# Performance work log

Hardware: AMD Instinct MI355X
Metric: run time of the kernel (lower is better)

The kernel has to match this reference:

```python
import jax, jax.numpy as jnp
import numpy as np

D_MODEL = 1024
D_FF = 4096
N_HEADS = 16
HEAD_DIM = D_MODEL // N_HEADS
EPS = 1e-6
B, S = 4, 2048


def _linear_params(key, d_in, d_out):
    kw, kb = jax.random.split(key)
    scale = 1.0 / np.sqrt(d_in)
    w = jax.random.uniform(kw, (d_in, d_out), minval=-scale, maxval=scale, dtype=jnp.float32)
    b = jax.random.uniform(kb, (d_out,), minval=-scale, maxval=scale, dtype=jnp.float32)
    return w, b


def setup_inputs() -> dict:
    key = jax.random.key(0)
    ks = jax.random.split(key, 16)
    x = jax.random.normal(ks[0], (B, S, D_MODEL), dtype=jnp.float32)
    enc = jax.random.normal(ks[1], (B, S, D_MODEL), dtype=jnp.float32)
    # masked self-attention params
    wq1, bq1 = _linear_params(ks[2], D_MODEL, D_MODEL)
    wk1, bk1 = _linear_params(ks[3], D_MODEL, D_MODEL)
    wv1, bv1 = _linear_params(ks[4], D_MODEL, D_MODEL)
    wo1, bo1 = _linear_params(ks[5], D_MODEL, D_MODEL)
    # cross-attention params
    wq2, bq2 = _linear_params(ks[6], D_MODEL, D_MODEL)
    wk2, bk2 = _linear_params(ks[7], D_MODEL, D_MODEL)
    wv2, bv2 = _linear_params(ks[8], D_MODEL, D_MODEL)
    wo2, bo2 = _linear_params(ks[9], D_MODEL, D_MODEL)
    # feed-forward params
    wf1, bf1 = _linear_params(ks[10], D_MODEL, D_FF)
    wf2, bf2 = _linear_params(ks[11], D_FF, D_MODEL)
    # layer norms
    g1 = jnp.ones((D_MODEL,), jnp.float32); be1 = jnp.zeros((D_MODEL,), jnp.float32)
    g2 = jnp.ones((D_MODEL,), jnp.float32); be2 = jnp.zeros((D_MODEL,), jnp.float32)
    g3 = jnp.ones((D_MODEL,), jnp.float32); be3 = jnp.zeros((D_MODEL,), jnp.float32)
    return dict(x=x, encoder_output=enc,
                wq1=wq1, bq1=bq1, wk1=wk1, bk1=bk1, wv1=wv1, bv1=bv1, wo1=wo1, bo1=bo1,
                wq2=wq2, bq2=bq2, wk2=wk2, bk2=bk2, wv2=wv2, bv2=bv2, wo2=wo2, bo2=bo2,
                wf1=wf1, bf1=bf1, wf2=wf2, bf2=bf2,
                g1=g1, be1=be1, g2=g2, be2=be2, g3=g3, be3=be3)


def _layer_norm(x, g, b):
    mu = jnp.mean(x, axis=-1, keepdims=True)
    var = jnp.mean(jnp.square(x - mu), axis=-1, keepdims=True)
    return (x - mu) * jax.lax.rsqrt(var + EPS) * g + b


def _mha(q_in, k_in, v_in, wq, bq, wk, bk, wv, bv, wo, bo, causal):
    b, s, _ = q_in.shape
    q = (q_in @ wq + bq).reshape(b, s, N_HEADS, HEAD_DIM)
    k = (k_in @ wk + bk).reshape(b, -1, N_HEADS, HEAD_DIM)
    v = (v_in @ wv + bv).reshape(b, -1, N_HEADS, HEAD_DIM)
    scores = jnp.einsum('bqhd,bkhd->bhqk', q, k) / np.sqrt(HEAD_DIM)
    if causal:
        mask = jnp.tril(jnp.ones((s, s), dtype=bool))
        scores = jnp.where(mask, scores, jnp.finfo(scores.dtype).min)
    attn = jax.nn.softmax(scores, axis=-1)
    out = jnp.einsum('bhqk,bkhd->bqhd', attn, v).reshape(b, s, D_MODEL)
    return out @ wo + bo


def reference(x, encoder_output,
              wq1, bq1, wk1, bk1, wv1, bv1, wo1, bo1,
              wq2, bq2, wk2, bk2, wv2, bv2, wo2, bo2,
              wf1, bf1, wf2, bf2,
              g1, be1, g2, be2, g3, be3):
    # masked self-attention + residual + LN
    residual = x
    x = _mha(x, x, x, wq1, bq1, wk1, bk1, wv1, bv1, wo1, bo1, causal=True)
    x = _layer_norm(x + residual, g1, be1)
    # cross-attention (note: q=enc, k=enc, v=x as in the original) + residual + LN
    residual = x
    x = _mha(encoder_output, encoder_output, x, wq2, bq2, wk2, bk2, wv2, bv2, wo2, bo2, causal=False)
    x = _layer_norm(x + residual, g2, be2)
    # feed-forward (dropout=0 -> identity in eval) + residual + LN
    residual = x
    x = jax.nn.relu(x @ wf1 + bf1) @ wf2 + bf2
    x = _layer_norm(x + residual, g3, be3)
    return x
```

## Files before the change

### kernel.cpp

```cpp
#include <hip/hip_runtime.h>


typedef _Float16 f16;
typedef _Float16 f16x8 __attribute__((ext_vector_type(8)));
typedef _Float16 f16x4 __attribute__((ext_vector_type(4)));
typedef __fp16 fp16x2 __attribute__((ext_vector_type(2)));
typedef float f32x4 __attribute__((ext_vector_type(4)));
typedef float f32x16 __attribute__((ext_vector_type(16)));
typedef unsigned int u32;

#define AS1 __attribute__((address_space(1)))
#define AS3 __attribute__((address_space(3)))

constexpr int S_LEN = 2048;
constexpr int DM    = 1024;

constexpr long OFF_W    = 0;
constexpr long OFF_XB   = 32L  << 20;
constexpr long OFF_ENC  = 48L  << 20;
constexpr long OFF_Q    = 64L  << 20;
constexpr long OFF_K    = 80L  << 20;
constexpr long OFF_V    = 96L  << 20;
constexpr long OFF_VT   = 112L << 20;
constexpr long OFF_AC   = 128L << 20;
constexpr long OFF_HID  = 144L << 20;
constexpr long OFF_F1   = 208L << 20;
constexpr long OFF_F2   = 240L << 20;
constexpr long OFF_F3   = 272L << 20;
constexpr long OFF_PART = 304L << 20;
constexpr long BUF_BYTES = 336L << 20;

__device__ alignas(4096) unsigned char g_buf[BUF_BYTES];

constexpr long WQ1T = OFF_W + (0L  << 20);
constexpr long WF1T = OFF_W + (16L << 20);
constexpr long WF2T = OFF_W + (24L << 20);
constexpr long WO1T = OFF_W + (6L  << 20);
constexpr long WQ2T = OFF_W + (8L  << 20);
constexpr long WV2T = OFF_W + (12L << 20);
constexpr long WO2T = OFF_W + (14L << 20);

__global__ __launch_bounds__(256) void cvt2_k(const float* __restrict__ x,
                                              const float* __restrict__ enc)
{
    const int bid = blockIdx.x;
    const bool second = bid >= 8192;
    const float* in = second ? enc : x;
    f16* out = (f16*)(g_buf + (second ? OFF_ENC : OFF_XB));
    long i = (long)(second ? bid - 8192 : bid) * 256 + threadIdx.x;
    float4 v = ((const float4*)in)[i];
    f16x4 h;
    h.x = (f16)v.x; h.y = (f16)v.y; h.z = (f16)v.z; h.w = (f16)v.w;
    *(f16x4*)(out + i * 4) = h;
}

struct TWJobs { const float* src[10]; };

__global__ __launch_bounds__(256) void transw_all_k(TWJobs jobs)
{
    __shared__ float t[32][33];
    const int bid = blockIdx.x;
    int j, local;
    if (bid < 8192)       { j = bid >> 10; local = bid & 1023; }
    else if (bid < 12288) { j = 8; local = bid - 8192; }
    else                  { j = 9; local = bid - 12288; }
    const int K = (j == 9) ? 4096 : 1024;
    const int N = (j == 8) ? 4096 : 1024;
    const int tnx = N >> 5;
    const int tx32 = local % tnx, ty32 = local / tnx;
    const long dstOff = (j < 8) ? (long)j * (2L << 20) : ((j == 8) ? WF1T : WF2T);
    const float* W = jobs.src[j];
    f16* Wt = (f16*)(g_buf + dstOff);

    int tx = threadIdx.x, ty = threadIdx.y;
    int c0 = tx32 * 32, r0 = ty32 * 32;
#pragma unroll
    for (int i = 0; i < 4; ++i)
        t[ty + 8*i][tx] = W[(long)(r0 + ty + 8*i) * N + c0 + tx];
    __syncthreads();
#pragma unroll
    for (int i = 0; i < 4; ++i)
        Wt[(long)(c0 + ty + 8*i) * K + r0 + tx] = (f16)t[tx][ty + 8*i];
}

template<int MODE>
__global__ __launch_bounds__(256) void gemm3_k(
    long aOff, long bOff, long cOff, long vtOff,
    const float* __restrict__ b0, const float* __restrict__ b1,
    const float* __restrict__ b2, const float* __restrict__ b3,
    int K, int lda, int ldb, int ldc, long chunkStride, int tvch)
{
    __shared__ alignas(16) f16 As[3][128 * 32];
    __shared__ alignas(16) f16 Bs[3][128 * 32];

    const int tid  = threadIdx.x;
    const int lane = tid & 63;
    const int w    = tid >> 6;
    const int cB   = lane & 15;
    const int hi   = lane >> 4;

    const int nwg = gridDim.x * gridDim.y;
    const int id  = blockIdx.y * gridDim.x + blockIdx.x;
    const int swz = (id & 7) * (nwg >> 3) + (id >> 3);
    const int bx  = swz % gridDim.x, by = swz / gridDim.x;
    const int row0 = by * 128, col0 = bx * 128;

    const f16* Ab = (const f16*)(g_buf + aOff);
    const f16* Bb = (const f16*)(g_buf + bOff);

    const int wr = (w >> 1) * 64;
    const int wc = (w & 1) * 64;

    f32x4 acc[4][4] = {};

    auto stage = [&](int buf, int kt) {
        const int kB = kt * 32;
        const int base = w * 64;
#pragma unroll
        for (int r = 0; r < 2; ++r) {
            const int idx  = r * 256 + base + lane;
            const int srow = idx >> 2, sb = idx & 3;
            const int gk = (sb ^ ((srow >> 1) & 3)) << 3;
            __builtin_amdgcn_global_load_lds(
                (const AS1 void*)(Ab + (long)(row0 + srow) * lda + kB + gk),
                (AS3 void*)(&As[buf][(r * 256 + base) * 8]), 16, 0, 0);
            __builtin_amdgcn_global_load_lds(
                (const AS1 void*)(Bb + (long)(col0 + srow) * ldb + kB + gk),
                (AS3 void*)(&Bs[buf][(r * 256 + base) * 8]), 16, 0, 0);
        }
    };

    const int nt = K >> 5;
    stage(0, 0);
    stage(1, 1);

    for (int t = 0; t < nt; ++t) {
        if (nt - t >= 2) asm volatile("s_waitcnt vmcnt(4)" ::: "memory");
        else             asm volatile("s_waitcnt vmcnt(0)" ::: "memory");
        __builtin_amdgcn_s_barrier();
        __builtin_amdgcn_sched_barrier(0);
        if (t + 2 < nt) stage((t + 2) % 3, t + 2);

        const int cur = t % 3;
        f16x8 af[4], bf[4];
#pragma unroll
        for (int m = 0; m < 4; ++m) {
            const int row = wr + m * 16 + cB;
            af[m] = *(const f16x8*)&As[cur][row * 32 + ((hi ^ ((row >> 1) & 3)) << 3)];
        }
#pragma unroll
        for (int n = 0; n < 4; ++n) {
            const int row = wc + n * 16 + cB;
            bf[n] = *(const f16x8*)&Bs[cur][row * 32 + ((hi ^ ((row >> 1) & 3)) << 3)];
        }
        __builtin_amdgcn_s_setprio(1);
#pragma unroll
        for (int m = 0; m < 4; ++m)
#pragma unroll
            for (int n = 0; n < 4; ++n)
                acc[m][n] = __builtin_amdgcn_mfma_f32_16x16x32_f16(af[m], bf[n], acc[m][n], 0, 0, 0);
        __builtin_amdgcn_s_setprio(0);
    }

    const int ch = col0 >> 10;
    const float* bp = (ch == 0) ? b0 : (ch == 1) ? b1 : (ch == 2) ? b2 : b3;

    if (MODE == 0 && ch == tvch) {
        f16* Vt = (f16*)(g_buf + vtOff);
#pragma unroll
        for (int m = 0; m < 4; ++m) {
#pragma unroll
            for (int n = 0; n < 4; ++n) {
                const int c = col0 + wc + n * 16 + cB;
                const int hh = (c >> 6) & 15, dd = c & 63;
                const float bv = bp[c & 1023];
                const int r0e = row0 + wr + m * 16 + hi * 4;
                const int bb = r0e >> 11, sS = r0e & 2047;
                f16x4 hv;
#pragma unroll
                for (int jj = 0; jj < 4; ++jj) hv[jj] = (f16)(acc[m][n][jj] + bv);
                *(f16x4*)(Vt + (((long)(bb * 16 + hh) * 64 + dd) * 2048 + sS)) = hv;
            }
        }
        return;
    }

    float* Cf = (float*)(g_buf + cOff);
    f16*  Ch = (f16*)(g_buf + cOff);
    const long cBase = (long)ch * chunkStride;
#pragma unroll
    for (int m = 0; m < 4; ++m) {
#pragma unroll
        for (int n = 0; n < 4; ++n) {
            const int c = col0 + wc + n * 16 + cB;
            const float bv = bp[c & 1023];
#pragma unroll
            for (int jj = 0; jj < 4; ++jj) {
                const int r = row0 + wr + m * 16 + hi * 4 + jj;
                float v = acc[m][n][jj] + bv;
                const long idx = cBase + (long)r * ldc + (c & 1023);
                if constexpr (MODE == 2) Cf[idx] = v;
                else                     Ch[idx] = (f16)v;
            }
        }
    }
}

template<int MODE>
__global__ __launch_bounds__(512, 1) void gemm8_k(
    long aOff, long bOff, long cOff, long partOff, long vtOff,
    const float* __restrict__ b0, const float* __restrict__ b1,
    const float* __restrict__ b2, const float* __restrict__ b3,
    int K, int lda, int ldb, int ldc, long chunkStride, int tvch)
{
    __shared__ alignas(16) f16 As[2][2][8192];
    __shared__ alignas(16) f16 Bs[2][2][8192];

    const int tid  = threadIdx.x;
    const int lane = tid & 63;
    const int w    = tid >> 6;
    const int cB   = lane & 15;
    const int hi   = lane >> 4;

    const int gx = gridDim.x, gy = gridDim.y;
    const int nwg = gx * gy * gridDim.z;
    const int id  = ((int)blockIdx.z * gy + (int)blockIdx.y) * gx + (int)blockIdx.x;
    const int swz = (id & 7) * (nwg >> 3) + (id >> 3);
    const int bx  = swz % gx;
    const int rem = swz / gx;
    const int by  = rem % gy;
    const int bz  = rem / gy;
    const int row0 = by * 256, col0 = bx * 256;

    const f16* Ab = (const f16*)(g_buf + aOff) + (long)bz * K;
    const f16* Bb = (const f16*)(g_buf + bOff) + (long)bz * K;

    const int wr = (w >> 2) * 128;
    const int wc = (w & 3) * 64;

    f32x4 acc[8][4] = {};

    auto stagePlane = [&](int buf, int kt, int mat, int kh) {
        const int kB = kt * 64 + kh * 32;
        const f16* src = mat ? Bb : Ab;
        const int ld   = mat ? ldb : lda;
        const int r0g  = mat ? col0 : row0;
        f16* dst = mat ? &Bs[buf][kh][0] : &As[buf][kh][0];
#pragma unroll
        for (int r = 0; r < 2; ++r) {
            const int idx  = r * 512 + w * 64 + lane;
            const int srow = idx >> 2, sb = idx & 3;
            const int gk = (sb ^ ((srow >> 1) & 3)) << 3;
            __builtin_amdgcn_global_load_lds(
                (const AS1 void*)(src + (long)(r0g + srow) * ld + kB + gk),
                (AS3 void*)(dst + (r * 512 + w * 64) * 8), 16, 0, 0);
        }
    };

    auto rdA = [&](int buf, int kh, int mf) -> f16x8 {
        const int row = wr + mf * 16 + cB;
        return *(const f16x8*)&As[buf][kh][row * 32 + ((hi ^ ((row >> 1) & 3)) << 3)];
    };
    auto rdB = [&](int buf, int kh, int nf) -> f16x8 {
        const int row = wc + nf * 16 + cB;
        return *(const f16x8*)&Bs[buf][kh][row * 32 + ((hi ^ ((row >> 1) & 3)) << 3)];
    };

    const int nt = K >> 6;
    stagePlane(0, 0, 0, 0);
    stagePlane(0, 0, 1, 0);
    stagePlane(0, 0, 0, 1);
    stagePlane(0, 0, 1, 1);

    for (int t = 0; t < nt; ++t) {
        const int cur = t & 1, nxt = cur ^ 1;
        const bool pf = (t + 1 < nt);
        f16x8 a[4], b[4];

        asm volatile("s_waitcnt vmcnt(4)" ::: "memory");
        __builtin_amdgcn_s_barrier();
        __builtin_amdgcn_sched_barrier(0);
#pragma unroll
        for (int n = 0; n < 4; ++n) b[n] = rdB(cur, 0, n);
#pragma unroll
        for (int m = 0; m < 4; ++m) a[m] = rdA(cur, 0, m);
        if (pf) stagePlane(nxt, t + 1, 0, 0);
        asm volatile("s_waitcnt lgkmcnt(0)" ::: "memory");
        __builtin_amdgcn_sched_barrier(0);
        __builtin_amdgcn_s_setprio(1);
#pragma unroll
        for (int m = 0; m < 4; ++m)
#pragma unroll
            for (int n = 0; n < 4; ++n)
                acc[m][n] = __builtin_amdgcn_mfma_f32_16x16x32_f16(a[m], b[n], acc[m][n], 0, 0, 0);
        __builtin_amdgcn_s_setprio(0);

        __builtin_amdgcn_s_barrier();
        __builtin_amdgcn_sched_barrier(0);
#pragma unroll
        for (int m = 0; m < 4; ++m) a[m] = rdA(cur, 0, m + 4);
        if (pf) stagePlane(nxt, t + 1, 1, 0);
        asm volatile("s_waitcnt lgkmcnt(0)" ::: "memory");
        __builtin_amdgcn_sched_barrier(0);
        __builtin_amdgcn_s_setprio(1);
#pragma unroll
        for (int m = 0; m < 4; ++m)
#pragma unroll
            for (int n = 0; n < 4; ++n)
                acc[4 + m][n] = __builtin_amdgcn_mfma_f32_16x16x32_f16(a[m], b[n], acc[4 + m][n], 0, 0, 0);
        __builtin_amdgcn_s_setprio(0);

        if (pf) asm volatile("s_waitcnt vmcnt(4)" ::: "memory");
        else    asm volatile("s_waitcnt vmcnt(0)" ::: "memory");
        __builtin_amdgcn_s_barrier();
        __builtin_amdgcn_sched_barrier(0);
#pragma unroll
        for (int n = 0; n < 4; ++n) b[n] = rdB(cur, 1, n);
#pragma unroll
        for (int m = 0; m < 4; ++m) a[m] = rdA(cur, 1, m);
        if (pf) stagePlane(nxt, t + 1, 0, 1);
        asm volatile("s_waitcnt lgkmcnt(0)" ::: "memory");
        __builtin_amdgcn_sched_barrier(0);
        __builtin_amdgcn_s_setprio(1);
#pragma unroll
        for (int m = 0; m < 4; ++m)
#pragma unroll
            for (int n = 0; n < 4; ++n)
                acc[m][n] = __builtin_amdgcn_mfma_f32_16x16x32_f16(a[m], b[n], acc[m][n], 0, 0, 0);
        __builtin_amdgcn_s_setprio(0);

        __builtin_amdgcn_s_barrier();
        __builtin_amdgcn_sched_barrier(0);
#pragma unroll
        for (int m = 0; m < 4; ++m) a[m] = rdA(cur, 1, m + 4);
        if (pf) stagePlane(nxt, t + 1, 1, 1);
        asm volatile("s_waitcnt lgkmcnt(0)" ::: "memory");
        __builtin_amdgcn_sched_barrier(0);
        __builtin_amdgcn_s_setprio(1);
#pragma unroll
        for (int m = 0; m < 4; ++m)
#pragma unroll
            for (int n = 0; n < 4; ++n)
                acc[4 + m][n] = __builtin_amdgcn_mfma_f32_16x16x32_f16(a[m], b[n], acc[4 + m][n], 0, 0, 0);
        __builtin_amdgcn_s_setprio(0);
    }

    const int ch = col0 >> 10;
    const float* bp = (ch == 0) ? b0 : (ch == 1) ? b1 : (ch == 2) ? b2 : b3;

    if (MODE == 0 && ch == tvch) {
        f16* Vt = (f16*)(g_buf + vtOff);
#pragma unroll
        for (int m = 0; m < 8; ++m) {
#pragma unroll
            for (int n = 0; n < 4; ++n) {
                const int c = col0 + wc + n * 16 + cB;
                const int hh = (c >> 6) & 15, dd = c & 63;
                const float bv = bp[c & 1023];
                const int r0e = row0 + wr + m * 16 + hi * 4;
                const int bb = r0e >> 11, sS = r0e & 2047;
                f16x4 hv;
#pragma unroll
                for (int jj = 0; jj < 4; ++jj) hv[jj] = (f16)(acc[m][n][jj] + bv);
                *(f16x4*)(Vt + (((long)(bb * 16 + hh) * 64 + dd) * 2048 + sS)) = hv;
            }
        }
        return;
    }

    float* Cf = (float*)(g_buf + (bz ? partOff : cOff));
    f16*  Ch = (f16*)(g_buf + cOff);
    const long cBase = (long)ch * chunkStride;
#pragma unroll
    for (int m = 0; m < 8; ++m) {
#pragma unroll
        for (int n = 0; n < 4; ++n) {
            const int c = col0 + wc + n * 16 + cB;
            const float bv = bz ? 0.f : bp[c & 1023];
#pragma unroll
            for (int jj = 0; jj < 4; ++jj) {
                const int r = row0 + wr + m * 16 + hi * 4 + jj;
                float v = acc[m][n][jj] + bv;
                if constexpr (MODE == 1) v = fmaxf(v, 0.f);
                const long idx = cBase + (long)r * ldc + (c & 1023);
                if constexpr (MODE == 2) Cf[idx] = v;
                else                     Ch[idx] = (f16)v;
            }
        }
    }
}

template<int CAUSAL>
__global__ __launch_bounds__(256, 4) void flash_k(long qOff, long kOff, long vtOff, long oOff)
{
    __shared__ alignas(16) f16 KV[2][2][4096];

    const int tid  = threadIdx.x;
    const int lane = tid & 63;
    const int w    = tid >> 6;
    const int ql   = lane & 31;
    const int s    = lane >> 5;

    int bh, pairIdx = 0, qtSingle = 0;
    if (CAUSAL) {
        const int raw   = (int)blockIdx.y * (int)gridDim.x + (int)blockIdx.x;
        const int newid = (raw & 7) * 64 + (raw >> 3);
        bh = newid >> 3; pairIdx = newid & 7;
    } else {
        const int raw   = (int)blockIdx.y * (int)gridDim.x + (int)blockIdx.x;
        const int newid = (raw & 7) * 128 + (raw >> 3);
        bh = newid >> 4; qtSingle = newid & 15;
    }

    const int b = bh >> 4, h = bh & 15;
    const long tokB = (long)b * S_LEN;

    const f16* Qb  = (const f16*)(g_buf + qOff);
    const f16* Kb  = (const f16*)(g_buf + kOff);
    const f16* Vtb = (const f16*)(g_buf + vtOff) + (long)bh * 64 * S_LEN;
    f16* Ob = (f16*)(g_buf + oOff);

    const int r8 = lane >> 3;
    const int c8 = lane & 7;
    const int sb = c8 ^ r8;

    auto stage = [&](int buf, int c) {
        const int kv0s = c * 64;
#pragma unroll
        for (int t = 0; t < 2; ++t) {
            const int grp = w * 2 + t;
            const int row = grp * 8 + r8;
            __builtin_amdgcn_global_load_lds(
                (const AS1 void*)(Kb + (tokB + kv0s + row) * DM + h * 64 + sb * 8),
                (AS3 void*)(&KV[buf][0][grp * 512]), 16, 0, 0);
            __builtin_amdgcn_global_load_lds(
                (const AS1 void*)(Vtb + (long)row * S_LEN + kv0s + sb * 8),
                (AS3 void*)(&KV[buf][1][grp * 512]), 16, 0, 0);
        }
    };

    const int npass = CAUSAL ? 2 : 1;
    for (int pass = 0; pass < npass; ++pass) {
        if (pass) {
            asm volatile("s_waitcnt lgkmcnt(0)" ::: "memory");
            __builtin_amdgcn_s_barrier();
        }
        const int qt  = CAUSAL ? (pass == 0 ? pairIdx : 15 - pairIdx) : qtSingle;
        const int q0  = qt * 128;
        const int nch = CAUSAL ? 2 * qt + 2 : (S_LEN / 64);

        f16x8 qf[4];
        {
            const f16 hs = (f16)(0.125f * 1.44269504088896f);
            const f16* qrow = Qb + (tokB + q0 + w * 32 + ql) * DM + h * 64 + s * 8;
#pragma unroll
            for (int kk = 0; kk < 4; ++kk) {
                qf[kk] = *(const f16x8*)(qrow + kk * 16);
#pragma unroll
                for (int i = 0; i < 8; ++i) qf[kk][i] = qf[kk][i] * hs;
            }
        }

        f32x16 oacc[2] = {};
        float lrow = 0.f;

        stage(0, 0);

        for (int c = 0; c < nch; ++c) {
            const int cur = c & 1;
            const int kv0 = c * 64;

            asm volatile("s_waitcnt vmcnt(0) lgkmcnt(0)" ::: "memory");
            __builtin_amdgcn_sched_barrier(0);
            __builtin_amdgcn_s_barrier();
            __builtin_amdgcn_sched_barrier(0);
            if (c + 1 < nch) stage(cur ^ 1, c + 1);

            const bool active = !CAUSAL || (kv0 <= q0 + w * 32 + 31);
            if (active) {
                f32x16 p[2] = {};
                __builtin_amdgcn_s_setprio(1);
#pragma unroll
                for (int kk = 0; kk < 4; ++kk) {
                    const int t16 = (kk * 2 + s) ^ (ql & 7);
                    f16x8 kf0 = *(const f16x8*)((const char*)&KV[cur][0][0] + ql * 128 + t16 * 16);
                    f16x8 kf1 = *(const f16x8*)((const char*)&KV[cur][0][0] + (32 + ql) * 128 + t16 * 16);
                    p[0] = __builtin_amdgcn_mfma_f32_32x32x16_f16(kf0, qf[kk], p[0], 0, 0, 0);
                    p[1] = __builtin_amdgcn_mfma_f32_32x32x16_f16(kf1, qf[kk], p[1], 0, 0, 0);
                }
                __builtin_amdgcn_s_setprio(0);

                if (CAUSAL && (kv0 + 63 > q0 + w * 32)) {
                    const int q = q0 + w * 32 + ql;
#pragma unroll
                    for (int v = 0; v < 2; ++v)
#pragma unroll
                        for (int r = 0; r < 16; ++r) {
                            const int kv = kv0 + v * 32 + (r & 3) + 8 * (r >> 2) + 4 * s;
                            if (kv > q) p[v][r] = -1e30f;
                        }
                }

                u32 pk[2][4][2];
                float rsum = 0.f;
#pragma unroll
                for (int v = 0; v < 2; ++v)
#pragma unroll
                    for (int a = 0; a < 4; ++a)
#pragma unroll
                        for (int cc = 0; cc < 2; ++cc) {
                            const float e0 = __builtin_amdgcn_exp2f(p[v][4 * a + 2 * cc] - 8.0f);
                            const float e1 = __builtin_amdgcn_exp2f(p[v][4 * a + 2 * cc + 1] - 8.0f);
                            rsum += e0 + e1;
                            union { fp16x2 h; u32 u; } cv;
                            cv.h = __builtin_amdgcn_cvt_pkrtz(e0, e1);
                            pk[v][a][cc] = cv.u;
                        }
                rsum += __shfl_xor(rsum, 32);
                lrow += rsum;

                u32 loc[2][2][2], exv[2][2][2];
#pragma unroll
                for (int v = 0; v < 2; ++v)
#pragma unroll
                    for (int k1 = 0; k1 < 2; ++k1)
#pragma unroll
                        for (int cc = 0; cc < 2; ++cc) {
                            const u32 pe = pk[v][2 * k1][cc];
                            const u32 po = pk[v][2 * k1 + 1][cc];
                            loc[v][k1][cc] = s ? po : pe;
                            const u32 snd = s ? pe : po;
                            exv[v][k1][cc] = (u32)__shfl_xor((int)snd, 32);
                        }

                __builtin_amdgcn_s_setprio(1);
#pragma unroll
                for (int ks = 0; ks < 4; ++ks) {
                    const int v = ks >> 1, k1 = ks & 1;
                    union { u32 u[4]; f16x8 hv; } pa;
                    pa.u[0] = s ? exv[v][k1][0] : loc[v][k1][0];
                    pa.u[1] = s ? exv[v][k1][1] : loc[v][k1][1];
                    pa.u[2] = s ? loc[v][k1][0] : exv[v][k1][0];
                    pa.u[3] = s ? loc[v][k1][1] : exv[v][k1][1];
                    const int tv = (ks * 2 + s) ^ (ql & 7);
                    f16x8 vf0 = *(const f16x8*)((const char*)&KV[cur][1][0] + ql * 128 + tv * 16);
                    f16x8 vf1 = *(const f16x8*)((const char*)&KV[cur][1][0] + (32 + ql) * 128 + tv * 16);
                    oacc[0] = __builtin_amdgcn_mfma_f32_32x32x16_f16(pa.hv, vf0, oacc[0], 0, 0, 0);
                    oacc[1] = __builtin_amdgcn_mfma_f32_32x32x16_f16(pa.hv, vf1, oacc[1], 0, 0, 0);
                }
                __builtin_amdgcn_s_setprio(0);
            }
        }

        asm volatile("s_waitcnt lgkmcnt(0)" ::: "memory");
        __builtin_amdgcn_sched_barrier(0);
        __builtin_amdgcn_s_barrier();

        f16* Es = ((f16*)&KV[0][0][0]) + w * 2304;
        const float linv = 1.0f / lrow;
#pragma unroll
        for (int r = 0; r < 16; ++r) {
            const int qr = (r & 3) + 8 * (r >> 2) + 4 * s;
            const float lb = __shfl(linv, qr);
            Es[qr * 72 + ql]      = (f16)(oacc[0][r] * lb);
            Es[qr * 72 + 32 + ql] = (f16)(oacc[1][r] * lb);
        }
        const int orow = lane >> 1;
        const int oh   = (lane & 1) * 32;
        const f16* srcp = ((const f16*)&KV[0][0][0]) + w * 2304 + orow * 72 + oh;
        f16* dst = Ob + (tokB + q0 + w * 32 + orow) * DM + h * 64 + oh;
#pragma unroll
        for (int t = 0; t < 4; ++t)
            *(f16x8*)(dst + t * 8) = *(const f16x8*)(srcp + t * 8);
    }
}

__global__ __launch_bounds__(256) void ln_k(
    long inOff, long in2Off, const float* __restrict__ residExt, long residOff,
    const float* __restrict__ gamma, const float* __restrict__ beta,
    float* __restrict__ outFExt, long outFOff, long outHOff)
{
    const float* in    = (const float*)(g_buf + inOff);
    const float* resid = residExt ? residExt : (const float*)(g_buf + residOff);
    float* outF = outFExt ? outFExt : (float*)(g_buf + outFOff);

    const long row = blockIdx.x;
    const int tid = threadIdx.x;
    const int lane = tid & 63, wid = tid >> 6;

    float4 a  = ((const float4*)(in    + row * DM))[tid];
    float4 rr = ((const float4*)(resid + row * DM))[tid];
    float x0 = a.x + rr.x, x1 = a.y + rr.y, x2 = a.z + rr.z, x3 = a.w + rr.w;
    if (in2Off >= 0) {
        const float* in2 = (const float*)(g_buf + in2Off);
        float4 p = ((const float4*)(in2 + row * DM))[tid];
        x0 += p.x; x1 += p.y; x2 += p.z; x3 += p.w;
    }

    __shared__ float red[4];
    float ss = x0 + x1 + x2 + x3;
#pragma unroll
    for (int o = 32; o > 0; o >>= 1) ss += __shfl_xor(ss, o);
    if (lane == 0) red[wid] = ss;
    __syncthreads();
    const float mu = (red[0] + red[1] + red[2] + red[3]) * (1.0f / DM);

    float d0 = x0 - mu, d1 = x1 - mu, d2 = x2 - mu, d3 = x3 - mu;
    float qq = d0*d0 + d1*d1 + d2*d2 + d3*d3;
#pragma unroll
    for (int o = 32; o > 0; o >>= 1) qq += __shfl_xor(qq, o);
    __syncthreads();
    if (lane == 0) red[wid] = qq;
    __syncthreads();
    const float var = (red[0] + red[1] + red[2] + red[3]) * (1.0f / DM);
    const float rs = rsqrtf(var + 1e-6f);

    float4 g  = ((const float4*)gamma)[tid];
    float4 be = ((const float4*)beta)[tid];
    float y0 = d0 * rs * g.x + be.x;
    float y1 = d1 * rs * g.y + be.y;
    float y2 = d2 * rs * g.z + be.z;
    float y3 = d3 * rs * g.w + be.w;

    ((float4*)(outF + row * DM))[tid] = make_float4(y0, y1, y2, y3);
    if (outHOff >= 0) {
        f16* outH = (f16*)(g_buf + outHOff);
        f16x4 hh; hh.x = (f16)y0; hh.y = (f16)y1; hh.z = (f16)y2; hh.w = (f16)y3;
        *(f16x4*)(outH + row * DM + tid * 4) = hh;
    }
}

extern "C" void kernel_launch(void* const* d_in, const int* in_sizes, int n_in,
                              void* d_out, int out_size, void* d_ws, size_t ws_size,
                              hipStream_t stream)
{
    (void)in_sizes; (void)n_in; (void)d_ws; (void)ws_size; (void)out_size;
    const float* x   = (const float*)d_in[0];
    const float* enc = (const float*)d_in[1];
    const float* wq1 = (const float*)d_in[2];  const float* bq1 = (const float*)d_in[3];
    const float* wk1 = (const float*)d_in[4];  const float* bk1 = (const float*)d_in[5];
    const float* wv1 = (const float*)d_in[6];  const float* bv1 = (const float*)d_in[7];
    const float* wo1 = (const float*)d_in[8];  const float* bo1 = (const float*)d_in[9];
    const float* wq2 = (const float*)d_in[10]; const float* bq2 = (const float*)d_in[11];
    const float* wk2 = (const float*)d_in[12]; const float* bk2 = (const float*)d_in[13];
    const float* wv2 = (const float*)d_in[14]; const float* bv2 = (const float*)d_in[15];
    const float* wo2 = (const float*)d_in[16]; const float* bo2 = (const float*)d_in[17];
    const float* wf1 = (const float*)d_in[18]; const float* bf1 = (const float*)d_in[19];
    const float* wf2 = (const float*)d_in[20]; const float* bf2 = (const float*)d_in[21];
    const float* g1  = (const float*)d_in[22]; const float* be1 = (const float*)d_in[23];
    const float* g2  = (const float*)d_in[24]; const float* be2 = (const float*)d_in[25];
    const float* g3  = (const float*)d_in[26]; const float* be3 = (const float*)d_in[27];
    float* out = (float*)d_out;

    const dim3 T256(256), T512(512), T32x8(32, 8);
    const long QKV_CHUNK = 8192L * 1024;

    cvt2_k<<<16384, T256, 0, stream>>>(x, enc);
    TWJobs jobs;
    jobs.src[0] = wq1; jobs.src[1] = wk1; jobs.src[2] = wv1; jobs.src[3] = wo1;
    jobs.src[4] = wq2; jobs.src[5] = wk2; jobs.src[6] = wv2; jobs.src[7] = wo2;
    jobs.src[8] = wf1; jobs.src[9] = wf2;
    transw_all_k<<<16384, T32x8, 0, stream>>>(jobs);

    gemm8_k<0><<<dim3(12, 32, 1), T512, 0, stream>>>(OFF_XB, WQ1T, OFF_Q, 0, OFF_VT,
        bq1, bk1, bv1, bv1, 1024, 1024, 1024, 1024, QKV_CHUNK, 2);
    flash_k<1><<<dim3(8, 64), T256, 0, stream>>>(OFF_Q, OFF_K, OFF_VT, OFF_AC);
    gemm3_k<2><<<dim3(8, 64), T256, 0, stream>>>(OFF_AC, WO1T, OFF_F2, 0,
        bo1, bo1, bo1, bo1, 1024, 1024, 1024, 1024, 1024, -1);
    ln_k<<<8192, T256, 0, stream>>>(OFF_F2, -1, x, 0, g1, be1, nullptr, OFF_F1, OFF_XB);

    gemm8_k<0><<<dim3(8, 32, 1), T512, 0, stream>>>(OFF_ENC, WQ2T, OFF_Q, 0, 0,
        bq2, bk2, bk2, bk2, 1024, 1024, 1024, 1024, QKV_CHUNK, -1);
    gemm3_k<0><<<dim3(8, 64), T256, 0, stream>>>(OFF_XB, WV2T, OFF_V, OFF_VT,
        bv2, bv2, bv2, bv2, 1024, 1024, 1024, 1024, 1024, 0);
    flash_k<0><<<dim3(16, 64), T256, 0, stream>>>(OFF_Q, OFF_K, OFF_VT, OFF_AC);
    gemm3_k<2><<<dim3(8, 64), T256, 0, stream>>>(OFF_AC, WO2T, OFF_F2, 0,
        bo2, bo2, bo2, bo2, 1024, 1024, 1024, 1024, 1024, -1);
    ln_k<<<8192, T256, 0, stream>>>(OFF_F2, -1, nullptr, OFF_F1, g2, be2, nullptr, OFF_F3, OFF_XB);

    gemm8_k<1><<<dim3(16, 32, 1), T512, 0, stream>>>(OFF_XB, WF1T, OFF_HID, 0, 0,
        bf1, bf1 + 1024, bf1 + 2048, bf1 + 3072, 1024, 1024, 1024, 4096, 1024, -1);
    gemm8_k<2><<<dim3(4, 32, 2), T512, 0, stream>>>(OFF_HID, WF2T, OFF_F2, OFF_PART, 0,
        bf2, bf2, bf2, bf2, 2048, 4096, 4096, 1024, 1024, -1);
    ln_k<<<8192, T256, 0, stream>>>(OFF_F2, OFF_PART, nullptr, OFF_F3, g3, be3, out, 0, -1);
}
```

Measured before the change: 622.1 us.

## Widen flash attention blocks to eight waves sharing each staged K/V tile

The flash attention kernel now runs 512-thread blocks. Two 128-row query tiles (the causal pair p and 15-p, or two adjacent tiles in cross-attention) are processed at once by eight waves that share one double-buffered K/V tile in LDS. This replaces the earlier sequential two-pass loop and halves the number of K/V loads per query tile. In the causal case waves working on the shorter tile go idle for the later chunks while still joining every barrier, and the larger block may lower occupancy.

```diff
diff --git a/kernel.cpp b/kernel.cpp
--- a/kernel.cpp
+++ b/kernel.cpp
@@ -391,9 +391,9 @@
 }
 
 template<int CAUSAL>
-__global__ __launch_bounds__(256, 4) void flash_k(long qOff, long kOff, long vtOff, long oOff)
+__global__ __launch_bounds__(512, 4) void flash_k(long qOff, long kOff, long vtOff, long oOff)
 {
-    __shared__ alignas(16) f16 KV[2][2][4096];
+    __shared__ alignas(16) f16 SH[18432];
 
     const int tid  = threadIdx.x;
     const int lane = tid & 63;
@@ -401,16 +401,14 @@
     const int ql   = lane & 31;
     const int s    = lane >> 5;
 
-    int bh, pairIdx = 0, qtSingle = 0;
-    if (CAUSAL) {
-        const int raw   = (int)blockIdx.y * (int)gridDim.x + (int)blockIdx.x;
-        const int newid = (raw & 7) * 64 + (raw >> 3);
-        bh = newid >> 3; pairIdx = newid & 7;
-    } else {
-        const int raw   = (int)blockIdx.y * (int)gridDim.x + (int)blockIdx.x;
-        const int newid = (raw & 7) * 128 + (raw >> 3);
-        bh = newid >> 4; qtSingle = newid & 15;
-    }
+    const int raw   = (int)blockIdx.y * (int)gridDim.x + (int)blockIdx.x;
+    const int newid = (raw & 7) * 64 + (raw >> 3);
+    const int bh    = newid >> 3;
+    const int p     = newid & 7;
+
+    const int qt  = CAUSAL ? ((w >> 2) ? 15 - p : p) : (2 * p + (w >> 2));
+    const int q0w = qt * 128 + (w & 3) * 32;
+    const int nch = CAUSAL ? (32 - 2 * p) : 32;
 
     const int b = bh >> 4, h = bh & 15;
     const long tokB = (long)b * S_LEN;
@@ -426,153 +424,141 @@
 
     auto stage = [&](int buf, int c) {
         const int kv0s = c * 64;
-#pragma unroll
-        for (int t = 0; t < 2; ++t) {
-            const int grp = w * 2 + t;
-            const int row = grp * 8 + r8;
-            __builtin_amdgcn_global_load_lds(
-                (const AS1 void*)(Kb + (tokB + kv0s + row) * DM + h * 64 + sb * 8),
-                (AS3 void*)(&KV[buf][0][grp * 512]), 16, 0, 0);
-            __builtin_amdgcn_global_load_lds(
-                (const AS1 void*)(Vtb + (long)row * S_LEN + kv0s + sb * 8),
-                (AS3 void*)(&KV[buf][1][grp * 512]), 16, 0, 0);
-        }
+        const int row  = w * 8 + r8;
+        __builtin_amdgcn_global_load_lds(
+            (const AS1 void*)(Kb + (tokB + kv0s + row) * DM + h * 64 + sb * 8),
+            (AS3 void*)(&SH[buf * 8192 + w * 512]), 16, 0, 0);
+        __builtin_amdgcn_global_load_lds(
+            (const AS1 void*)(Vtb + (long)row * S_LEN + kv0s + sb * 8),
+            (AS3 void*)(&SH[buf * 8192 + 4096 + w * 512]), 16, 0, 0);
     };
 
-    const int npass = CAUSAL ? 2 : 1;
-    for (int pass = 0; pass < npass; ++pass) {
-        if (pass) {
-            asm volatile("s_waitcnt lgkmcnt(0)" ::: "memory");
-            __builtin_amdgcn_s_barrier();
-        }
-        const int qt  = CAUSAL ? (pass == 0 ? pairIdx : 15 - pairIdx) : qtSingle;
-        const int q0  = qt * 128;
-        const int nch = CAUSAL ? 2 * qt + 2 : (S_LEN / 64);
-
-        f16x8 qf[4];
-        {
-            const f16 hs = (f16)(0.125f * 1.44269504088896f);
-            const f16* qrow = Qb + (tokB + q0 + w * 32 + ql) * DM + h * 64 + s * 8;
+    stage(0, 0);
+
+    f16x8 qf[4];
+    {
+        const f16 hs = (f16)(0.125f * 1.44269504088896f);
+        const f16* qrow = Qb + (tokB + q0w + ql) * DM + h * 64 + s * 8;
+#pragma unroll
+        for (int kk = 0; kk < 4; ++kk) {
+            qf[kk] = *(const f16x8*)(qrow + kk * 16);
+#pragma unroll
+            for (int i = 0; i < 8; ++i) qf[kk][i] = qf[kk][i] * hs;
+        }
+    }
+
+    f32x16 oacc[2] = {};
+    float lrow = 0.f;
+
+    for (int c = 0; c < nch; ++c) {
+        const int cur = c & 1;
+        const int kv0 = c * 64;
+
+        asm volatile("s_waitcnt vmcnt(0) lgkmcnt(0)" ::: "memory");
+        __builtin_amdgcn_sched_barrier(0);
+        __builtin_amdgcn_s_barrier();
+        __builtin_amdgcn_sched_barrier(0);
+        if (c + 1 < nch) stage(cur ^ 1, c + 1);
+
+        const bool active = !CAUSAL || (kv0 <= q0w + 31);
+        if (active) {
+            const char* Kl = (const char*)SH + cur * 16384;
+            const char* Vl = Kl + 8192;
+
+            f32x16 pr[2] = {};
+            __builtin_amdgcn_s_setprio(1);
 #pragma unroll
             for (int kk = 0; kk < 4; ++kk) {
-                qf[kk] = *(const f16x8*)(qrow + kk * 16);
-#pragma unroll
-                for (int i = 0; i < 8; ++i) qf[kk][i] = qf[kk][i] * hs;
+                const int t16 = (kk * 2 + s) ^ (ql & 7);
+                f16x8 kf0 = *(const f16x8*)(Kl + ql * 128 + t16 * 16);
+                f16x8 kf1 = *(const f16x8*)(Kl + (32 + ql) * 128 + t16 * 16);
+                pr[0] = __builtin_amdgcn_mfma_f32_32x32x16_f16(kf0, qf[kk], pr[0], 0, 0, 0);
+                pr[1] = __builtin_amdgcn_mfma_f32_32x32x16_f16(kf1, qf[kk], pr[1], 0, 0, 0);
             }
-        }
-
-        f32x16 oacc[2] = {};
-        float lrow = 0.f;
-
-        stage(0, 0);
-
-        for (int c = 0; c < nch; ++c) {
-            const int cur = c & 1;
-            const int kv0 = c * 64;
-
-            asm volatile("s_waitcnt vmcnt(0) lgkmcnt(0)" ::: "memory");
-            __builtin_amdgcn_sched_barrier(0);
-            __builtin_amdgcn_s_barrier();
-            __builtin_amdgcn_sched_barrier(0);
-            if (c + 1 < nch) stage(cur ^ 1, c + 1);
-
-            const bool active = !CAUSAL || (kv0 <= q0 + w * 32 + 31);
-            if (active) {
-                f32x16 p[2] = {};
-                __builtin_amdgcn_s_setprio(1);
-#pragma unroll
-                for (int kk = 0; kk < 4; ++kk) {
-                    const int t16 = (kk * 2 + s) ^ (ql & 7);
-                    f16x8 kf0 = *(const f16x8*)((const char*)&KV[cur][0][0] + ql * 128 + t16 * 16);
-                    f16x8 kf1 = *(const f16x8*)((const char*)&KV[cur][0][0] + (32 + ql) * 128 + t16 * 16);
-                    p[0] = __builtin_amdgcn_mfma_f32_32x32x16_f16(kf0, qf[kk], p[0], 0, 0, 0);
-                    p[1] = __builtin_amdgcn_mfma_f32_32x32x16_f16(kf1, qf[kk], p[1], 0, 0, 0);
-                }
-                __builtin_amdgcn_s_setprio(0);
-
-                if (CAUSAL && (kv0 + 63 > q0 + w * 32)) {
-                    const int q = q0 + w * 32 + ql;
-#pragma unroll
-                    for (int v = 0; v < 2; ++v)
-#pragma unroll
-                        for (int r = 0; r < 16; ++r) {
-                            const int kv = kv0 + v * 32 + (r & 3) + 8 * (r >> 2) + 4 * s;
-                            if (kv > q) p[v][r] = -1e30f;
-                        }
-                }
-
-                u32 pk[2][4][2];
-                float rsum = 0.f;
+            __builtin_amdgcn_s_setprio(0);
+
+            if (CAUSAL && (kv0 + 63 > q0w)) {
+                const int q = q0w + ql;
 #pragma unroll
                 for (int v = 0; v < 2; ++v)
 #pragma unroll
-                    for (int a = 0; a < 4; ++a)
-#pragma unroll
-                        for (int cc = 0; cc < 2; ++cc) {
-                            const float e0 = __builtin_amdgcn_exp2f(p[v][4 * a + 2 * cc] - 8.0f);
-                            const float e1 = __builtin_amdgcn_exp2f(p[v][4 * a + 2 * cc + 1] - 8.0f);
-                            rsum += e0 + e1;
-                            union { fp16x2 h; u32 u; } cv;
-                            cv.h = __builtin_amdgcn_cvt_pkrtz(e0, e1);
-                            pk[v][a][cc] = cv.u;
-                        }
-                rsum += __shfl_xor(rsum, 32);
-                lrow += rsum;
-
-                u32 loc[2][2][2], exv[2][2][2];
-#pragma unroll
-                for (int v = 0; v < 2; ++v)
-#pragma unroll
-                    for (int k1 = 0; k1 < 2; ++k1)
-#pragma unroll
-                        for (int cc = 0; cc < 2; ++cc) {
-                            const u32 pe = pk[v][2 * k1][cc];
-                            const u32 po = pk[v][2 * k1 + 1][cc];
-                            loc[v][k1][cc] = s ? po : pe;
-                            const u32 snd = s ? pe : po;
-                            exv[v][k1][cc] = (u32)__shfl_xor((int)snd, 32);
-                        }
-
-                __builtin_amdgcn_s_setprio(1);
-#pragma unroll
-                for (int ks = 0; ks < 4; ++ks) {
-                    const int v = ks >> 1, k1 = ks & 1;
-                    union { u32 u[4]; f16x8 hv; } pa;
-                    pa.u[0] = s ? exv[v][k1][0] : loc[v][k1][0];
-                    pa.u[1] = s ? exv[v][k1][1] : loc[v][k1][1];
-                    pa.u[2] = s ? loc[v][k1][0] : exv[v][k1][0];
-                    pa.u[3] = s ? loc[v][k1][1] : exv[v][k1][1];
-                    const int tv = (ks * 2 + s) ^ (ql & 7);
-                    f16x8 vf0 = *(const f16x8*)((const char*)&KV[cur][1][0] + ql * 128 + tv * 16);
-                    f16x8 vf1 = *(const f16x8*)((const char*)&KV[cur][1][0] + (32 + ql) * 128 + tv * 16);
-                    oacc[0] = __builtin_amdgcn_mfma_f32_32x32x16_f16(pa.hv, vf0, oacc[0], 0, 0, 0);
-                    oacc[1] = __builtin_amdgcn_mfma_f32_32x32x16_f16(pa.hv, vf1, oacc[1], 0, 0, 0);
-                }
-                __builtin_amdgcn_s_setprio(0);
+                    for (int r = 0; r < 16; ++r) {
+                        const int kv = kv0 + v * 32 + (r & 3) + 8 * (r >> 2) + 4 * s;
+                        if (kv > q) pr[v][r] = -1e30f;
+                    }
             }
-        }
-
-        asm volatile("s_waitcnt lgkmcnt(0)" ::: "memory");
-        __builtin_amdgcn_sched_barrier(0);
-        __builtin_amdgcn_s_barrier();
-
-        f16* Es = ((f16*)&KV[0][0][0]) + w * 2304;
-        const float linv = 1.0f / lrow;
-#pragma unroll
-        for (int r = 0; r < 16; ++r) {
-            const int qr = (r & 3) + 8 * (r >> 2) + 4 * s;
-            const float lb = __shfl(linv, qr);
-            Es[qr * 72 + ql]      = (f16)(oacc[0][r] * lb);
-            Es[qr * 72 + 32 + ql] = (f16)(oacc[1][r] * lb);
-        }
-        const int orow = lane >> 1;
-        const int oh   = (lane & 1) * 32;
-        const f16* srcp = ((const f16*)&KV[0][0][0]) + w * 2304 + orow * 72 + oh;
-        f16* dst = Ob + (tokB + q0 + w * 32 + orow) * DM + h * 64 + oh;
-#pragma unroll
-        for (int t = 0; t < 4; ++t)
-            *(f16x8*)(dst + t * 8) = *(const f16x8*)(srcp + t * 8);
-    }
+
+            u32 pk[2][4][2];
+            float rsum = 0.f;
+#pragma unroll
+            for (int v = 0; v < 2; ++v)
+#pragma unroll
+                for (int a = 0; a < 4; ++a)
+#pragma unroll
+                    for (int cc = 0; cc < 2; ++cc) {
+                        const float e0 = __builtin_amdgcn_exp2f(pr[v][4 * a + 2 * cc] - 8.0f);
+                        const float e1 = __builtin_amdgcn_exp2f(pr[v][4 * a + 2 * cc + 1] - 8.0f);
+                        rsum += e0 + e1;
+                        union { fp16x2 h; u32 u; } cv;
+                        cv.h = __builtin_amdgcn_cvt_pkrtz(e0, e1);
+                        pk[v][a][cc] = cv.u;
+                    }
+            rsum += __shfl_xor(rsum, 32);
+            lrow += rsum;
+
+            u32 loc[2][2][2], exv[2][2][2];
+#pragma unroll
+            for (int v = 0; v < 2; ++v)
+#pragma unroll
+                for (int k1 = 0; k1 < 2; ++k1)
+#pragma unroll
+                    for (int cc = 0; cc < 2; ++cc) {
+                        const u32 pe = pk[v][2 * k1][cc];
+                        const u32 po = pk[v][2 * k1 + 1][cc];
+                        loc[v][k1][cc] = s ? po : pe;
+                        const u32 snd = s ? pe : po;
+                        exv[v][k1][cc] = (u32)__shfl_xor((int)snd, 32);
+                    }
+
+            __builtin_amdgcn_s_setprio(1);
+#pragma unroll
+            for (int ks = 0; ks < 4; ++ks) {
+                const int v = ks >> 1, k1 = ks & 1;
+                union { u32 u[4]; f16x8 hv; } pa;
+                pa.u[0] = s ? exv[v][k1][0] : loc[v][k1][0];
+                pa.u[1] = s ? exv[v][k1][1] : loc[v][k1][1];
+                pa.u[2] = s ? loc[v][k1][0] : exv[v][k1][0];
+                pa.u[3] = s ? loc[v][k1][1] : exv[v][k1][1];
+                const int tv = (ks * 2 + s) ^ (ql & 7);
+                f16x8 vf0 = *(const f16x8*)(Vl + ql * 128 + tv * 16);
+                f16x8 vf1 = *(const f16x8*)(Vl + (32 + ql) * 128 + tv * 16);
+                oacc[0] = __builtin_amdgcn_mfma_f32_32x32x16_f16(pa.hv, vf0, oacc[0], 0, 0, 0);
+                oacc[1] = __builtin_amdgcn_mfma_f32_32x32x16_f16(pa.hv, vf1, oacc[1], 0, 0, 0);
+            }
+            __builtin_amdgcn_s_setprio(0);
+        }
+    }
+
+    asm volatile("s_waitcnt lgkmcnt(0)" ::: "memory");
+    __builtin_amdgcn_sched_barrier(0);
+    __builtin_amdgcn_s_barrier();
+
+    f16* Es = SH + w * 2304;
+    const float linv = 1.0f / lrow;
+#pragma unroll
+    for (int r = 0; r < 16; ++r) {
+        const int qr = (r & 3) + 8 * (r >> 2) + 4 * s;
+        const float lb = __shfl(linv, qr);
+        Es[qr * 72 + ql]      = (f16)(oacc[0][r] * lb);
+        Es[qr * 72 + 32 + ql] = (f16)(oacc[1][r] * lb);
+    }
+    const int orow = lane >> 1;
+    const int oh   = (lane & 1) * 32;
+    const f16* srcp = Es + orow * 72 + oh;
+    f16* dst = Ob + (tokB + q0w + orow) * DM + h * 64 + oh;
+#pragma unroll
+    for (int t = 0; t < 4; ++t)
+        *(f16x8*)(dst + t * 8) = *(const f16x8*)(srcp + t * 8);
 }
 
 __global__ __launch_bounds__(256) void ln_k(
@@ -664,7 +650,7 @@
 
     gemm8_k<0><<<dim3(12, 32, 1), T512, 0, stream>>>(OFF_XB, WQ1T, OFF_Q, 0, OFF_VT,
         bq1, bk1, bv1, bv1, 1024, 1024, 1024, 1024, QKV_CHUNK, 2);
-    flash_k<1><<<dim3(8, 64), T256, 0, stream>>>(OFF_Q, OFF_K, OFF_VT, OFF_AC);
+    flash_k<1><<<dim3(8, 64), T512, 0, stream>>>(OFF_Q, OFF_K, OFF_VT, OFF_AC);
     gemm3_k<2><<<dim3(8, 64), T256, 0, stream>>>(OFF_AC, WO1T, OFF_F2, 0,
         bo1, bo1, bo1, bo1, 1024, 1024, 1024, 1024, 1024, -1);
     ln_k<<<8192, T256, 0, stream>>>(OFF_F2, -1, x, 0, g1, be1, nullptr, OFF_F1, OFF_XB);
@@ -673,7 +659,7 @@
         bq2, bk2, bk2, bk2, 1024, 1024, 1024, 1024, QKV_CHUNK, -1);
     gemm3_k<0><<<dim3(8, 64), T256, 0, stream>>>(OFF_XB, WV2T, OFF_V, OFF_VT,
         bv2, bv2, bv2, bv2, 1024, 1024, 1024, 1024, 1024, 0);
-    flash_k<0><<<dim3(16, 64), T256, 0, stream>>>(OFF_Q, OFF_K, OFF_VT, OFF_AC);
+    flash_k<0><<<dim3(8, 64), T512, 0, stream>>>(OFF_Q, OFF_K, OFF_VT, OFF_AC);
     gemm3_k<2><<<dim3(8, 64), T256, 0, stream>>>(OFF_AC, WO2T, OFF_F2, 0,
         bo2, bo2, bo2, bo2, 1024, 1024, 1024, 1024, 1024, -1);
     ln_k<<<8192, T256, 0, stream>>>(OFF_F2, -1, nullptr, OFF_F1, g2, be2, nullptr, OFF_F3, OFF_XB);
```

Result: faster. 596.1 us (-4.2%).
